# Kernel tuning notes

Measured on AMD Instinct MI355X. Metric: run time of the kernel, lower is better.

## Reference

```python
import jax, jax.numpy as jnp
import numpy as np

B, N, M = 4, 8192, 8192


def setup_inputs() -> dict:
    key = jax.random.key(0)
    k1, k2, k3, k4 = jax.random.split(key, 4)
    xyz1 = jax.random.normal(k1, (B, N, 3), dtype=jnp.float32)
    xyz2 = jax.random.normal(k2, (B, M, 3), dtype=jnp.float32)
    weights1 = jax.random.uniform(k3, (B, N), dtype=jnp.float32)
    weights2 = jax.random.uniform(k4, (B, M), dtype=jnp.float32)
    return {"xyz1": xyz1, "xyz2": xyz2, "weights1": weights1, "weights2": weights2}


def _chamfer_dists(xyz1, xyz2):
    # Squared L2 pairwise distances via the ||a||^2 + ||b||^2 - 2 a.b identity
    # (avoids materializing a [B, N, M, 3] difference tensor).
    sq1 = jnp.sum(xyz1 * xyz1, axis=-1)            # [B, N]
    sq2 = jnp.sum(xyz2 * xyz2, axis=-1)            # [B, M]
    dots = jnp.einsum("bnc,bmc->bnm", xyz1, xyz2)  # [B, N, M]
    d = sq1[:, :, None] + sq2[:, None, :] - 2.0 * dots
    d = jnp.maximum(d, 0.0)
    dist1 = jnp.min(d, axis=2)  # [B, N] nearest in xyz2 for each point in xyz1
    dist2 = jnp.min(d, axis=1)  # [B, M] nearest in xyz1 for each point in xyz2
    return dist1, dist2


def reference(xyz1, xyz2, weights1, weights2):
    dist1, dist2 = _chamfer_dists(xyz1, xyz2)
    dist1 = dist1 * weights1
    dist2 = dist2 * weights2
    dist1_avg = jnp.sum(dist1) / jnp.sum(weights1)
    dist2_avg = jnp.sum(dist2) / jnp.sum(weights2)
    return (dist1_avg + dist2_avg) / 2.0
```

## Files before the change

kernel.cpp:

```cpp
#include <hip/hip_runtime.h>

#define TPB 256
#define TPBM 512
constexpr int Bsz  = 4;
constexpr int Npts = 8192;
constexpr int Mpts = 8192;
constexpr int PTS  = Bsz * Npts;
constexpr int QT_PER_B = Npts / 16;
constexpr int CT_PER_B = Mpts / 16;
constexpr int RBLK = 64;

typedef __attribute__((ext_vector_type(8))) short short8;
typedef __attribute__((ext_vector_type(4))) float f32x4;

__device__ __forceinline__ float min3f(float a, float b, float c) {
    return fminf(fminf(a, b), c);
}

__device__ __forceinline__ void mfma2_bf16(const short8& a0, const short8& a1,
                                           const short8& b,
                                           f32x4& d0, f32x4& d1) {
    asm("v_mfma_f32_16x16x32_bf16 %0, %2, %4, 0\n\t"
        "v_mfma_f32_16x16x32_bf16 %1, %3, %4, 0\n\t"
        "s_nop 7\n\t"
        "s_nop 3"
        : "=&v"(d0), "=&v"(d1)
        : "v"(a0), "v"(a1), "v"(b));
}

__device__ __forceinline__ unsigned short bfh(float v) {
    unsigned u = __float_as_uint(v);
    return (unsigned short)((u + 0x7fffu + ((u >> 16) & 1u)) >> 16);
}
__device__ __forceinline__ float b2f(unsigned short h) {
    return __uint_as_float(((unsigned)h) << 16);
}
__device__ __forceinline__ void split3(float v, unsigned short& h,
                                       unsigned short& m, unsigned short& l) {
    h = bfh(v); float fh = b2f(h);
    m = bfh(v - fh); float fm = b2f(m);
    l = bfh(v - fh - fm);
}

__device__ __forceinline__ unsigned short pickA(int o, unsigned short h,
                                                unsigned short m, unsigned short l) {
    return o < 3 ? h : (o < 5 ? m : l);
}
__device__ __forceinline__ unsigned short pickB(int o, unsigned short h,
                                                unsigned short m, unsigned short l) {
    return (o == 1 || o == 4) ? m : (o == 2 ? l : h);
}

__global__ void __launch_bounds__(TPB) prep_kernel(
    const float* __restrict__ xyz1, const float* __restrict__ xyz2,
    short* __restrict__ aQ, short* __restrict__ bC)
{
    int id   = blockIdx.x * TPB + threadIdx.x;
    int side = id >> 17;
    int tl   = id & 131071;
    int tile = tl >> 6, lane = tl & 63;
    int r = lane & 15, g = lane >> 4;

    const float* src = side ? xyz2 : xyz1;
    int p = tile * 16 + r;
    float x = src[p * 3 + 0], y = src[p * 3 + 1], z = src[p * 3 + 2];
    float n = fmaf(x, x, fmaf(y, y, z * z));
    float s = side ? 1.f : -2.f;

    unsigned short xh, xm, xl, yh, ym, yl, zh, zm, zl, nh, nm, nl;
    split3(s * x, xh, xm, xl);
    split3(s * y, yh, ym, yl);
    split3(s * z, zh, zm, zl);
    split3(n, nh, nm, nl);
    const unsigned short ONE = 0x3F80;

    short8 v;
#pragma unroll
    for (int j = 0; j < 8; ++j) {
        int k = g * 8 + j;
        unsigned short u = 0;
        if (k < 18) {
            int c = k / 6, o = k - 6 * c;
            unsigned short h = c == 0 ? xh : (c == 1 ? yh : zh);
            unsigned short m = c == 0 ? xm : (c == 1 ? ym : zm);
            unsigned short l = c == 0 ? xl : (c == 1 ? yl : zl);
            u = side ? pickB(o, h, m, l) : pickA(o, h, m, l);
        } else if (k < 21) {
            u = side ? ONE : (k == 18 ? nh : (k == 19 ? nm : nl));
        } else if (k < 24) {
            u = side ? (k == 21 ? nh : (k == 22 ? nm : nl)) : ONE;
        }
        v[j] = (short)u;
    }
    short8* dst = (short8*)(side ? bC : aQ);
    dst[tile * 64 + lane] = v;
}

__global__ void __launch_bounds__(TPBM, 8) chamfer_mfma_kernel(
    const short* __restrict__ aQ, const short* __restrict__ bC,
    unsigned int* __restrict__ partials)
{
    int bid = blockIdx.x;
    int linear = (bid & 7) * 128 + (bid >> 3);
    int batch = linear >> 8;
    int rem = linear & 255;
    int qs = rem >> 3;
    int cs = rem & 7;
    int w = threadIdx.x >> 6, lane = threadIdx.x & 63;

    int qtile0 = batch * QT_PER_B + qs * 16 + w * 2;
    int ctile0 = batch * CT_PER_B + cs * 64;

    const short8* aT = (const short8*)aQ;
    const short8* bT = (const short8*)bC;

    __shared__ unsigned int colb[1024];
    colb[threadIdx.x]       = 0x7f7fffffu;
    colb[threadIdx.x + 512] = 0x7f7fffffu;

    short8 a0 = aT[(qtile0 + 0) * 64 + lane];
    short8 a1 = aT[(qtile0 + 1) * 64 + lane];

    const f32x4 inf4 = {3.4e38f, 3.4e38f, 3.4e38f, 3.4e38f};
    f32x4 rowp0 = inf4, rowp1 = inf4;
    __syncthreads();

    const short8* bP = bT + ctile0 * 64 + lane;
    unsigned int* mycol = &colb[lane & 15];

    short8 b0 = bP[0], b1;

#pragma unroll 2
    for (int ct = 0; ct < 64; ct += 2) {
        b1 = bP[(ct + 1) * 64];
        {
            f32x4 d0, d1;
            mfma2_bf16(a0, a1, b0, d0, d1);
            rowp0 = __builtin_elementwise_min(rowp0, d0);
            rowp1 = __builtin_elementwise_min(rowp1, d1);
            float ca = min3f(d0[0], d0[1], d0[2]);
            ca = min3f(ca, d0[3], d1[0]);
            ca = min3f(ca, d1[1], d1[2]);
            ca = fminf(ca, d1[3]);
            atomicMin(mycol + ct * 16, __float_as_uint(fmaxf(ca, 0.f)));
        }
        b0 = bP[(ct + 2) * 64];
        {
            f32x4 d0, d1;
            mfma2_bf16(a0, a1, b1, d0, d1);
            rowp0 = __builtin_elementwise_min(rowp0, d0);
            rowp1 = __builtin_elementwise_min(rowp1, d1);
            float ca = min3f(d0[0], d0[1], d0[2]);
            ca = min3f(ca, d0[3], d1[0]);
            ca = min3f(ca, d1[1], d1[2]);
            ca = fminf(ca, d1[3]);
            atomicMin(mycol + (ct + 1) * 16, __float_as_uint(fmaxf(ca, 0.f)));
        }
    }

#pragma unroll
    for (int t = 0; t < 2; ++t) {
        f32x4 rp = t ? rowp1 : rowp0;
#pragma unroll
        for (int i = 0; i < 4; ++i) {
            float v = rp[i];
            v = fminf(v, __shfl_xor(v, 1));
            v = fminf(v, __shfl_xor(v, 2));
            v = fminf(v, __shfl_xor(v, 4));
            v = fminf(v, __shfl_xor(v, 8));
            if ((lane & 15) == 0) {
                int q = (qtile0 + t) * 16 + (lane >> 4) * 4 + i;
                atomicMin(&partials[q], __float_as_uint(fmaxf(v, 0.f)));
            }
        }
    }

    __syncthreads();
    int cbase = PTS + ctile0 * 16;
    atomicMin(&partials[cbase + threadIdx.x],       colb[threadIdx.x]);
    atomicMin(&partials[cbase + threadIdx.x + 512], colb[threadIdx.x + 512]);
}

__global__ void __launch_bounds__(TPB) reduce_kernel(
    const float* __restrict__ partials,
    const float* __restrict__ w1, const float* __restrict__ w2,
    float2* __restrict__ slots)
{
    int gid = blockIdx.x * TPB + threadIdx.x;
    int dir = gid >> 13;
    int idx = gid & 8191;
    const float4* d4 = (const float4*)(partials + (size_t)dir * PTS);
    const float4* w4 = (const float4*)(dir ? w2 : w1);
    float4 d = d4[idx], w = w4[idx];
    float c = d.x * w.x + d.y * w.y + d.z * w.z + d.w * w.w;
    float s = w.x + w.y + w.z + w.w;

    for (int off = 32; off; off >>= 1) {
        c += __shfl_down(c, off);
        s += __shfl_down(s, off);
    }
    __shared__ float sc[4], ss[4];
    int lane = threadIdx.x & 63, wid = threadIdx.x >> 6;
    if (lane == 0) { sc[wid] = c; ss[wid] = s; }
    __syncthreads();
    if (threadIdx.x == 0) {
        slots[blockIdx.x] =
            make_float2(sc[0] + sc[1] + sc[2] + sc[3],
                        ss[0] + ss[1] + ss[2] + ss[3]);
    }
}

__global__ void __launch_bounds__(64) final_kernel(
    const float2* __restrict__ slots, float* __restrict__ out)
{
    float2 v = slots[threadIdx.x];
    for (int off = 16; off; off >>= 1) {
        v.x += __shfl_down(v.x, off, 32);
        v.y += __shfl_down(v.y, off, 32);
    }
    float c1 = __shfl(v.x, 32), s1 = __shfl(v.y, 32);
    if (threadIdx.x == 0)
        out[0] = 0.5f * (v.x / v.y + c1 / s1);
}

extern "C" void kernel_launch(void* const* d_in, const int* in_sizes, int n_in,
                              void* d_out, int out_size, void* d_ws, size_t ws_size,
                              hipStream_t stream) {
    const float* xyz1 = (const float*)d_in[0];
    const float* xyz2 = (const float*)d_in[1];
    const float* w1   = (const float*)d_in[2];
    const float* w2   = (const float*)d_in[3];
    float* out = (float*)d_out;

    unsigned int* partials = (unsigned int*)d_ws;
    float2* slots = (float2*)((char*)d_ws + (size_t)2 * PTS * sizeof(unsigned int));
    short* aQ = (short*)((char*)d_ws + (1u << 20));
    short* bC = (short*)((char*)d_ws + (4u << 20));

    prep_kernel<<<1024, TPB, 0, stream>>>(xyz1, xyz2, aQ, bC);
    chamfer_mfma_kernel<<<1024, TPBM, 0, stream>>>(aQ, bC, partials);
    reduce_kernel<<<RBLK, TPB, 0, stream>>>((const float*)partials, w1, w2, slots);
    final_kernel<<<1, 64, 0, stream>>>(slots, out);
}
```

Measured before the change: 94.88 us.

## Process four query tiles per wave with smaller column chunks and blocks

Each wave now holds four A query tiles instead of two and issues four MFMAs per loaded B tile, so each B load and each LDS column atomicMin covers twice as many query rows. Blocks shrink to 256 threads, each covering 32 column tiles, and the grid doubles to 2048 blocks. Launch bounds change to 5 blocks per SM. The aim is to cut B-tile global loads and LDS atomics per MFMA. The cost is more live accumulator registers, which may lower occupancy, plus more global row atomics.

Measured after the change: 118.3 us. 1.25x slower.

```diff
diff --git a/kernel.cpp b/kernel.cpp
--- a/kernel.cpp
+++ b/kernel.cpp
@@ -1,7 +1,6 @@
 #include <hip/hip_runtime.h>
 
 #define TPB 256
-#define TPBM 512
 constexpr int Bsz  = 4;
 constexpr int Npts = 8192;
 constexpr int Mpts = 8192;
@@ -17,15 +16,19 @@
     return fminf(fminf(a, b), c);
 }
 
-__device__ __forceinline__ void mfma2_bf16(const short8& a0, const short8& a1,
+__device__ __forceinline__ void mfma4_bf16(const short8& a0, const short8& a1,
+                                           const short8& a2, const short8& a3,
                                            const short8& b,
-                                           f32x4& d0, f32x4& d1) {
-    asm("v_mfma_f32_16x16x32_bf16 %0, %2, %4, 0\n\t"
-        "v_mfma_f32_16x16x32_bf16 %1, %3, %4, 0\n\t"
+                                           f32x4& d0, f32x4& d1,
+                                           f32x4& d2, f32x4& d3) {
+    asm("v_mfma_f32_16x16x32_bf16 %0, %4, %8, 0\n\t"
+        "v_mfma_f32_16x16x32_bf16 %1, %5, %8, 0\n\t"
+        "v_mfma_f32_16x16x32_bf16 %2, %6, %8, 0\n\t"
+        "v_mfma_f32_16x16x32_bf16 %3, %7, %8, 0\n\t"
         "s_nop 7\n\t"
         "s_nop 3"
-        : "=&v"(d0), "=&v"(d1)
-        : "v"(a0), "v"(a1), "v"(b));
+        : "=&v"(d0), "=&v"(d1), "=&v"(d2), "=&v"(d3)
+        : "v"(a0), "v"(a1), "v"(a2), "v"(a3), "v"(b));
 }
 
 __device__ __forceinline__ unsigned short bfh(float v) {
@@ -96,33 +99,35 @@
     dst[tile * 64 + lane] = v;
 }
 
-__global__ void __launch_bounds__(TPBM, 8) chamfer_mfma_kernel(
+__global__ void __launch_bounds__(TPB, 5) chamfer_mfma_kernel(
     const short* __restrict__ aQ, const short* __restrict__ bC,
     unsigned int* __restrict__ partials)
 {
     int bid = blockIdx.x;
-    int linear = (bid & 7) * 128 + (bid >> 3);
-    int batch = linear >> 8;
-    int rem = linear & 255;
-    int qs = rem >> 3;
-    int cs = rem & 7;
+    int linear = (bid & 7) * 256 + (bid >> 3);
+    int batch = linear >> 9;
+    int rem = linear & 511;
+    int qs = rem >> 4;
+    int cs = rem & 15;
     int w = threadIdx.x >> 6, lane = threadIdx.x & 63;
 
-    int qtile0 = batch * QT_PER_B + qs * 16 + w * 2;
-    int ctile0 = batch * CT_PER_B + cs * 64;
+    int qtile0 = batch * QT_PER_B + qs * 16 + w * 4;
+    int ctile0 = batch * CT_PER_B + cs * 32;
 
     const short8* aT = (const short8*)aQ;
     const short8* bT = (const short8*)bC;
 
-    __shared__ unsigned int colb[1024];
+    __shared__ unsigned int colb[512];
     colb[threadIdx.x]       = 0x7f7fffffu;
-    colb[threadIdx.x + 512] = 0x7f7fffffu;
+    colb[threadIdx.x + 256] = 0x7f7fffffu;
 
     short8 a0 = aT[(qtile0 + 0) * 64 + lane];
     short8 a1 = aT[(qtile0 + 1) * 64 + lane];
+    short8 a2 = aT[(qtile0 + 2) * 64 + lane];
+    short8 a3 = aT[(qtile0 + 3) * 64 + lane];
 
     const f32x4 inf4 = {3.4e38f, 3.4e38f, 3.4e38f, 3.4e38f};
-    f32x4 rowp0 = inf4, rowp1 = inf4;
+    f32x4 rowp0 = inf4, rowp1 = inf4, rowp2 = inf4, rowp3 = inf4;
     __syncthreads();
 
     const short8* bP = bT + ctile0 * 64 + lane;
@@ -131,36 +136,51 @@
     short8 b0 = bP[0], b1;
 
 #pragma unroll 2
-    for (int ct = 0; ct < 64; ct += 2) {
+    for (int ct = 0; ct < 32; ct += 2) {
         b1 = bP[(ct + 1) * 64];
         {
-            f32x4 d0, d1;
-            mfma2_bf16(a0, a1, b0, d0, d1);
+            f32x4 d0, d1, d2, d3;
+            mfma4_bf16(a0, a1, a2, a3, b0, d0, d1, d2, d3);
             rowp0 = __builtin_elementwise_min(rowp0, d0);
             rowp1 = __builtin_elementwise_min(rowp1, d1);
+            rowp2 = __builtin_elementwise_min(rowp2, d2);
+            rowp3 = __builtin_elementwise_min(rowp3, d3);
             float ca = min3f(d0[0], d0[1], d0[2]);
             ca = min3f(ca, d0[3], d1[0]);
             ca = min3f(ca, d1[1], d1[2]);
             ca = fminf(ca, d1[3]);
-            atomicMin(mycol + ct * 16, __float_as_uint(fmaxf(ca, 0.f)));
-        }
+            float cb = min3f(d2[0], d2[1], d2[2]);
+            cb = min3f(cb, d2[3], d3[0]);
+            cb = min3f(cb, d3[1], d3[2]);
+            cb = fminf(cb, d3[3]);
+            atomicMin(mycol + ct * 16, __float_as_uint(fmaxf(fminf(ca, cb), 0.f)));
+        }
+        asm volatile("" : "+v"(rowp0), "+v"(rowp1), "+v"(rowp2), "+v"(rowp3));
+
         b0 = bP[(ct + 2) * 64];
         {
-            f32x4 d0, d1;
-            mfma2_bf16(a0, a1, b1, d0, d1);
+            f32x4 d0, d1, d2, d3;
+            mfma4_bf16(a0, a1, a2, a3, b1, d0, d1, d2, d3);
             rowp0 = __builtin_elementwise_min(rowp0, d0);
             rowp1 = __builtin_elementwise_min(rowp1, d1);
+            rowp2 = __builtin_elementwise_min(rowp2, d2);
+            rowp3 = __builtin_elementwise_min(rowp3, d3);
             float ca = min3f(d0[0], d0[1], d0[2]);
             ca = min3f(ca, d0[3], d1[0]);
             ca = min3f(ca, d1[1], d1[2]);
             ca = fminf(ca, d1[3]);
-            atomicMin(mycol + (ct + 1) * 16, __float_as_uint(fmaxf(ca, 0.f)));
-        }
+            float cb = min3f(d2[0], d2[1], d2[2]);
+            cb = min3f(cb, d2[3], d3[0]);
+            cb = min3f(cb, d3[1], d3[2]);
+            cb = fminf(cb, d3[3]);
+            atomicMin(mycol + (ct + 1) * 16, __float_as_uint(fmaxf(fminf(ca, cb), 0.f)));
+        }
+        asm volatile("" : "+v"(rowp0), "+v"(rowp1), "+v"(rowp2), "+v"(rowp3));
     }
 
 #pragma unroll
-    for (int t = 0; t < 2; ++t) {
-        f32x4 rp = t ? rowp1 : rowp0;
+    for (int t = 0; t < 4; ++t) {
+        f32x4 rp = t == 0 ? rowp0 : (t == 1 ? rowp1 : (t == 2 ? rowp2 : rowp3));
 #pragma unroll
         for (int i = 0; i < 4; ++i) {
             float v = rp[i];
@@ -178,7 +198,7 @@
     __syncthreads();
     int cbase = PTS + ctile0 * 16;
     atomicMin(&partials[cbase + threadIdx.x],       colb[threadIdx.x]);
-    atomicMin(&partials[cbase + threadIdx.x + 512], colb[threadIdx.x + 512]);
+    atomicMin(&partials[cbase + threadIdx.x + 256], colb[threadIdx.x + 256]);
 }
 
 __global__ void __launch_bounds__(TPB) reduce_kernel(
@@ -238,7 +258,7 @@
     short* bC = (short*)((char*)d_ws + (4u << 20));
 
     prep_kernel<<<1024, TPB, 0, stream>>>(xyz1, xyz2, aQ, bC);
-    chamfer_mfma_kernel<<<1024, TPBM, 0, stream>>>(aQ, bC, partials);
+    chamfer_mfma_kernel<<<2048, TPB, 0, stream>>>(aQ, bC, partials);
     reduce_kernel<<<RBLK, TPB, 0, stream>>>((const float*)partials, w1, w2, slots);
     final_kernel<<<1, 64, 0, stream>>>(slots, out);
 }
```

## Switch to 32x32x16 bf16 MFMA with two-term coordinate split

Applied to the files above, without the earlier changes.

The distance tile is now computed with one 32x32x16 bf16 MFMA per wave instead of two 16x16x32 MFMAs. To fit in K=16, coordinates are split into hi/mid bf16 parts (dropping the low term and the lo*hi cross products) while the norms keep a three-term split. The goal is to halve the MFMA count and the per-tile atomic and reduction overhead by covering a larger output tile per instruction. The cost is lower precision in the dot-product term, which could shift the result relative to the fp32 reference.

Measured after the change: 97.06 us. 1.02x slower.

```diff
diff --git a/kernel.cpp b/kernel.cpp
--- a/kernel.cpp
+++ b/kernel.cpp
@@ -6,26 +6,25 @@
 constexpr int Npts = 8192;
 constexpr int Mpts = 8192;
 constexpr int PTS  = Bsz * Npts;
-constexpr int QT_PER_B = Npts / 16;
-constexpr int CT_PER_B = Mpts / 16;
+constexpr int QT_PER_B = Npts / 32;
+constexpr int CT_PER_B = Mpts / 32;
 constexpr int RBLK = 64;
 
-typedef __attribute__((ext_vector_type(8))) short short8;
-typedef __attribute__((ext_vector_type(4))) float f32x4;
+typedef __attribute__((ext_vector_type(8)))  short short8;
+typedef __attribute__((ext_vector_type(16))) float f32x16;
 
 __device__ __forceinline__ float min3f(float a, float b, float c) {
     return fminf(fminf(a, b), c);
 }
 
-__device__ __forceinline__ void mfma2_bf16(const short8& a0, const short8& a1,
-                                           const short8& b,
-                                           f32x4& d0, f32x4& d1) {
-    asm("v_mfma_f32_16x16x32_bf16 %0, %2, %4, 0\n\t"
-        "v_mfma_f32_16x16x32_bf16 %1, %3, %4, 0\n\t"
+__device__ __forceinline__ f32x16 mfma_32x32(short8 a, short8 b) {
+    f32x16 d;
+    asm("v_mfma_f32_32x32x16_bf16 %0, %1, %2, 0\n\t"
+        "s_nop 7\n\t"
         "s_nop 7\n\t"
         "s_nop 3"
-        : "=&v"(d0), "=&v"(d1)
-        : "v"(a0), "v"(a1), "v"(b));
+        : "=&v"(d) : "v"(a), "v"(b));
+    return d;
 }
 
 __device__ __forceinline__ unsigned short bfh(float v) {
@@ -34,6 +33,10 @@
 }
 __device__ __forceinline__ float b2f(unsigned short h) {
     return __uint_as_float(((unsigned)h) << 16);
+}
+__device__ __forceinline__ void split2(float v, unsigned short& h,
+                                       unsigned short& m) {
+    h = bfh(v); m = bfh(v - b2f(h));
 }
 __device__ __forceinline__ void split3(float v, unsigned short& h,
                                        unsigned short& m, unsigned short& l) {
@@ -42,35 +45,26 @@
     l = bfh(v - fh - fm);
 }
 
-__device__ __forceinline__ unsigned short pickA(int o, unsigned short h,
-                                                unsigned short m, unsigned short l) {
-    return o < 3 ? h : (o < 5 ? m : l);
-}
-__device__ __forceinline__ unsigned short pickB(int o, unsigned short h,
-                                                unsigned short m, unsigned short l) {
-    return (o == 1 || o == 4) ? m : (o == 2 ? l : h);
-}
-
 __global__ void __launch_bounds__(TPB) prep_kernel(
     const float* __restrict__ xyz1, const float* __restrict__ xyz2,
     short* __restrict__ aQ, short* __restrict__ bC)
 {
     int id   = blockIdx.x * TPB + threadIdx.x;
-    int side = id >> 17;
-    int tl   = id & 131071;
+    int side = id >> 16;
+    int tl   = id & 65535;
     int tile = tl >> 6, lane = tl & 63;
-    int r = lane & 15, g = lane >> 4;
+    int r = lane & 31, g = lane >> 5;
 
     const float* src = side ? xyz2 : xyz1;
-    int p = tile * 16 + r;
+    int p = tile * 32 + r;
     float x = src[p * 3 + 0], y = src[p * 3 + 1], z = src[p * 3 + 2];
     float n = fmaf(x, x, fmaf(y, y, z * z));
     float s = side ? 1.f : -2.f;
 
-    unsigned short xh, xm, xl, yh, ym, yl, zh, zm, zl, nh, nm, nl;
-    split3(s * x, xh, xm, xl);
-    split3(s * y, yh, ym, yl);
-    split3(s * z, zh, zm, zl);
+    unsigned short xh, xm, yh, ym, zh, zm, nh, nm, nl;
+    split2(s * x, xh, xm);
+    split2(s * y, yh, ym);
+    split2(s * z, zh, zm);
     split3(n, nh, nm, nl);
     const unsigned short ONE = 0x3F80;
 
@@ -79,16 +73,16 @@
     for (int j = 0; j < 8; ++j) {
         int k = g * 8 + j;
         unsigned short u = 0;
-        if (k < 18) {
-            int c = k / 6, o = k - 6 * c;
+        if (k < 9) {
+            int c = k / 3, o = k - 3 * c;
             unsigned short h = c == 0 ? xh : (c == 1 ? yh : zh);
             unsigned short m = c == 0 ? xm : (c == 1 ? ym : zm);
-            unsigned short l = c == 0 ? xl : (c == 1 ? yl : zl);
-            u = side ? pickB(o, h, m, l) : pickA(o, h, m, l);
-        } else if (k < 21) {
-            u = side ? ONE : (k == 18 ? nh : (k == 19 ? nm : nl));
-        } else if (k < 24) {
-            u = side ? (k == 21 ? nh : (k == 22 ? nm : nl)) : ONE;
+            u = side ? (o == 1 ? m : h)
+                     : (o < 2 ? h : m);
+        } else if (k < 12) {
+            u = side ? ONE : (k == 9 ? nh : (k == 10 ? nm : nl));
+        } else if (k < 15) {
+            u = side ? (k == 12 ? nh : (k == 13 ? nm : nl)) : ONE;
         }
         v[j] = (short)u;
     }
@@ -108,8 +102,8 @@
     int cs = rem & 7;
     int w = threadIdx.x >> 6, lane = threadIdx.x & 63;
 
-    int qtile0 = batch * QT_PER_B + qs * 16 + w * 2;
-    int ctile0 = batch * CT_PER_B + cs * 64;
+    int qtile  = batch * QT_PER_B + qs * 8 + w;
+    int ctile0 = batch * CT_PER_B + cs * 32;
 
     const short8* aT = (const short8*)aQ;
     const short8* bT = (const short8*)bC;
@@ -118,65 +112,69 @@
     colb[threadIdx.x]       = 0x7f7fffffu;
     colb[threadIdx.x + 512] = 0x7f7fffffu;
 
-    short8 a0 = aT[(qtile0 + 0) * 64 + lane];
-    short8 a1 = aT[(qtile0 + 1) * 64 + lane];
-
-    const f32x4 inf4 = {3.4e38f, 3.4e38f, 3.4e38f, 3.4e38f};
-    f32x4 rowp0 = inf4, rowp1 = inf4;
+    short8 a = aT[qtile * 64 + lane];
+
+    f32x16 rowp;
+#pragma unroll
+    for (int i = 0; i < 16; ++i) rowp[i] = 3.4e38f;
     __syncthreads();
 
     const short8* bP = bT + ctile0 * 64 + lane;
-    unsigned int* mycol = &colb[lane & 15];
+    unsigned int* mycol = &colb[lane & 31];
 
     short8 b0 = bP[0], b1;
 
 #pragma unroll 2
-    for (int ct = 0; ct < 64; ct += 2) {
+    for (int ct = 0; ct < 32; ct += 2) {
         b1 = bP[(ct + 1) * 64];
         {
-            f32x4 d0, d1;
-            mfma2_bf16(a0, a1, b0, d0, d1);
-            rowp0 = __builtin_elementwise_min(rowp0, d0);
-            rowp1 = __builtin_elementwise_min(rowp1, d1);
-            float ca = min3f(d0[0], d0[1], d0[2]);
-            ca = min3f(ca, d0[3], d1[0]);
-            ca = min3f(ca, d1[1], d1[2]);
-            ca = fminf(ca, d1[3]);
-            atomicMin(mycol + ct * 16, __float_as_uint(fmaxf(ca, 0.f)));
+            f32x16 d = mfma_32x32(a, b0);
+            rowp = __builtin_elementwise_min(rowp, d);
+            float ca = min3f(d[0], d[1], d[2]);
+            ca = min3f(ca, d[3], d[4]);
+            ca = min3f(ca, d[5], d[6]);
+            ca = fminf(ca, d[7]);
+            float cb = min3f(d[8], d[9], d[10]);
+            cb = min3f(cb, d[11], d[12]);
+            cb = min3f(cb, d[13], d[14]);
+            cb = fminf(cb, d[15]);
+            atomicMin(mycol + ct * 32,
+                      __float_as_uint(fmaxf(fminf(ca, cb), 0.f)));
         }
         b0 = bP[(ct + 2) * 64];
         {
-            f32x4 d0, d1;
-            mfma2_bf16(a0, a1, b1, d0, d1);
-            rowp0 = __builtin_elementwise_min(rowp0, d0);
-            rowp1 = __builtin_elementwise_min(rowp1, d1);
-            float ca = min3f(d0[0], d0[1], d0[2]);
-            ca = min3f(ca, d0[3], d1[0]);
-            ca = min3f(ca, d1[1], d1[2]);
-            ca = fminf(ca, d1[3]);
-            atomicMin(mycol + (ct + 1) * 16, __float_as_uint(fmaxf(ca, 0.f)));
+            f32x16 d = mfma_32x32(a, b1);
+            rowp = __builtin_elementwise_min(rowp, d);
+            float ca = min3f(d[0], d[1], d[2]);
+            ca = min3f(ca, d[3], d[4]);
+            ca = min3f(ca, d[5], d[6]);
+            ca = fminf(ca, d[7]);
+            float cb = min3f(d[8], d[9], d[10]);
+            cb = min3f(cb, d[11], d[12]);
+            cb = min3f(cb, d[13], d[14]);
+            cb = fminf(cb, d[15]);
+            atomicMin(mycol + (ct + 1) * 32,
+                      __float_as_uint(fmaxf(fminf(ca, cb), 0.f)));
         }
     }
 
 #pragma unroll
-    for (int t = 0; t < 2; ++t) {
-        f32x4 rp = t ? rowp1 : rowp0;
-#pragma unroll
-        for (int i = 0; i < 4; ++i) {
-            float v = rp[i];
-            v = fminf(v, __shfl_xor(v, 1));
-            v = fminf(v, __shfl_xor(v, 2));
-            v = fminf(v, __shfl_xor(v, 4));
-            v = fminf(v, __shfl_xor(v, 8));
-            if ((lane & 15) == 0) {
-                int q = (qtile0 + t) * 16 + (lane >> 4) * 4 + i;
-                atomicMin(&partials[q], __float_as_uint(fmaxf(v, 0.f)));
-            }
+    for (int i = 0; i < 16; ++i) {
+        float v = rowp[i];
+        v = fminf(v, __shfl_xor(v, 1));
+        v = fminf(v, __shfl_xor(v, 2));
+        v = fminf(v, __shfl_xor(v, 4));
+        v = fminf(v, __shfl_xor(v, 8));
+        v = fminf(v, __shfl_xor(v, 16));
+        if ((lane & 31) == 0) {
+            int row = (i & 3) + 4 * (lane >> 5) + 8 * (i >> 2);
+            atomicMin(&partials[qtile * 32 + row],
+                      __float_as_uint(fmaxf(v, 0.f)));
         }
     }
 
     __syncthreads();
-    int cbase = PTS + ctile0 * 16;
+    int cbase = PTS + ctile0 * 32;
     atomicMin(&partials[cbase + threadIdx.x],       colb[threadIdx.x]);
     atomicMin(&partials[cbase + threadIdx.x + 512], colb[threadIdx.x + 512]);
 }
@@ -237,7 +235,7 @@
     short* aQ = (short*)((char*)d_ws + (1u << 20));
     short* bC = (short*)((char*)d_ws + (4u << 20));
 
-    prep_kernel<<<1024, TPB, 0, stream>>>(xyz1, xyz2, aQ, bC);
+    prep_kernel<<<512, TPB, 0, stream>>>(xyz1, xyz2, aQ, bC);
     chamfer_mfma_kernel<<<1024, TPBM, 0, stream>>>(aQ, bC, partials);
     reduce_kernel<<<RBLK, TPB, 0, stream>>>((const float*)partials, w1, w2, slots);
     final_kernel<<<1, 64, 0, stream>>>(slots, out);
```
